# Kernel optimization log

Measured on AMD Instinct MI355X. Metric: run time of the kernel, lower is better.

## Reference

```python
import jax, jax.numpy as jnp
import numpy as np


def _lstm_cell(x, h, c, W_ih, b_ih, W_hh, b_hh):
    # PyTorch gate order: i, f, g, o
    gates = x @ W_ih.T + b_ih + h @ W_hh.T + b_hh
    i, f, g, o = jnp.split(gates, 4, axis=-1)
    c = jax.nn.sigmoid(f) * c + jax.nn.sigmoid(i) * jnp.tanh(g)
    h = jax.nn.sigmoid(o) * jnp.tanh(c)
    return h, c


def setup_inputs() -> dict:
    key = jax.random.key(0)
    ks = jax.random.split(key, 12)
    B, CR, PR = 8192, 168, 24
    E, I, H = 20, 3, 40  # embedding_size, input_size, hidden_size
    s = 0.1
    return {
        "z1": jax.random.normal(ks[0], (B, CR, 1), jnp.float32),
        "xc": jax.random.normal(ks[1], (B, CR + PR, I), jnp.float32),
        "W_emb": jax.random.normal(ks[2], (E, 1), jnp.float32) * s,
        "b_emb": jax.random.normal(ks[3], (E,), jnp.float32) * s,
        "W_ih": jax.random.normal(ks[4], (4 * H, E + I), jnp.float32) * s,
        "b_ih": jax.random.normal(ks[5], (4 * H,), jnp.float32) * s,
        "W_hh": jax.random.normal(ks[6], (4 * H, H), jnp.float32) * s,
        "b_hh": jax.random.normal(ks[7], (4 * H,), jnp.float32) * s,
        "W_mu": jax.random.normal(ks[8], (1, H), jnp.float32) * s,
        "b_mu": jax.random.normal(ks[9], (1,), jnp.float32) * s,
        "W_sig": jax.random.normal(ks[10], (1, H), jnp.float32) * s,
        "b_sig": jax.random.normal(ks[11], (1,), jnp.float32) * s,
        "conditioning_range": 168,
        "prediction_range": 24,
    }


def reference(z1, xc, W_emb, b_emb, W_ih, b_ih, W_hh, b_hh, W_mu, b_mu, W_sig, b_sig, conditioning_range, prediction_range):
    B = z1.shape[0]
    H = W_hh.shape[1]
    v = jnp.mean(z1, axis=1, keepdims=True) + 1.0  # [B,1,1] scale factor
    v2 = v[:, 0, :]                                # [B,1]

    # ---- conditioning phase: t = 1 .. CR-1 ----
    emb_cond = (z1[:, : conditioning_range - 1, :] / v) @ W_emb.T + b_emb  # [B,CR-1,E]
    xs = jnp.concatenate([emb_cond, xc[:, 1:conditioning_range, :]], axis=-1)
    xs = jnp.swapaxes(xs, 0, 1)  # [T,B,E+I]
    h0 = jnp.zeros((B, H), z1.dtype)
    c0 = jnp.zeros((B, H), z1.dtype)

    def cond_step(carry, x_t):
        h, c = carry
        h, c = _lstm_cell(x_t, h, c, W_ih, b_ih, W_hh, b_hh)
        return (h, c), None

    (h, c), _ = jax.lax.scan(cond_step, (h0, c0), xs)

    eps = jax.random.normal(jax.random.key(42), (prediction_range, B, 1), z1.dtype)
    xc_pred = jnp.swapaxes(
        xc[:, conditioning_range: conditioning_range + prediction_range, :], 0, 1
    )  # [PR,B,I]

    def pred_step(carry, inp):
        h, c, y = carry
        x_t, e_t = inp
        emb = (y / v2) @ W_emb.T + b_emb                       # [B,E]
        h, c = _lstm_cell(jnp.concatenate([emb, x_t], axis=-1), h, c, W_ih, b_ih, W_hh, b_hh)
        mu = h @ W_mu.T + b_mu                                 # [B,1]
        sigma = jax.nn.softplus(h @ W_sig.T + b_sig)           # [B,1]
        y = jax.lax.stop_gradient(mu + sigma * e_t)            # Normal.sample (no grad)
        return (h, c, y), (y * v2, mu * v2, sigma * v2)

    y0 = z1[:, -1, :]  # [B,1]
    _, (outs, mus, sigmas) = jax.lax.scan(pred_step, (h, c, y0), (xc_pred, eps))

    outputs = jnp.swapaxes(outs, 0, 1)[..., :]   # [B,PR,1]
    mus = jnp.swapaxes(mus, 0, 1)
    sigmas = jnp.swapaxes(sigmas, 0, 1)
    return outputs, mus, sigmas
```

## Files before the change

### kernel.cpp

```cpp
#include <hip/hip_runtime.h>

#define B_TOTAL   8192
#define CR_LEN    168
#define PR_LEN    24
#define HID       40
#define ROWS      6
#define NTHREADS  256
#define OUT_STRIDE (B_TOTAL * PR_LEN)

__device__ __forceinline__ float fast_rcp(float x) { return __builtin_amdgcn_rcpf(x); }

__device__ __forceinline__ float sigmoid_f(float x) {
    return fast_rcp(1.0f + __expf(-x));
}

__device__ __forceinline__ float tanh_f(float x) {
    float ax = fabsf(x);
    float e  = __expf(-2.0f * ax);
    float r  = (1.0f - e) * fast_rcp(1.0f + e);
    return copysignf(r, x);
}

__device__ __forceinline__ unsigned rotl32(unsigned x, int d) {
    return (x << d) | (x >> (32 - d));
}

__device__ __forceinline__ void threefry2x32(unsigned k0, unsigned k1,
                                             unsigned c0, unsigned c1,
                                             unsigned& o0, unsigned& o1) {
    const unsigned k2 = 0x1BD11BDAu ^ k0 ^ k1;
    unsigned x0 = c0 + k0, x1 = c1 + k1;
#define TF_R(rr) { x0 += x1; x1 = rotl32(x1, (rr)); x1 ^= x0; }
    TF_R(13) TF_R(15) TF_R(26) TF_R(6)  x0 += k1; x1 += k2 + 1u;
    TF_R(17) TF_R(29) TF_R(16) TF_R(24) x0 += k2; x1 += k0 + 2u;
    TF_R(13) TF_R(15) TF_R(26) TF_R(6)  x0 += k0; x1 += k1 + 3u;
    TF_R(17) TF_R(29) TF_R(16) TF_R(24) x0 += k1; x1 += k2 + 4u;
    TF_R(13) TF_R(15) TF_R(26) TF_R(6)  x0 += k2; x1 += k0 + 5u;
#undef TF_R
    o0 = x0; o1 = x1;
}

__device__ __forceinline__ float erfinv_f(float x) {
    float w = -__logf(fmaf(-x, x, 1.0f));
    float p;
    if (w < 5.0f) {
        w -= 2.5f;
        p = 2.81022636e-08f;
        p = fmaf(p, w, 3.43273939e-07f);
        p = fmaf(p, w, -3.5233877e-06f);
        p = fmaf(p, w, -4.39150654e-06f);
        p = fmaf(p, w, 0.00021858087f);
        p = fmaf(p, w, -0.00125372503f);
        p = fmaf(p, w, -0.00417768164f);
        p = fmaf(p, w, 0.246640727f);
        p = fmaf(p, w, 1.50140941f);
    } else {
        w = sqrtf(w) - 3.0f;
        p = -0.000200214257f;
        p = fmaf(p, w, 0.000100950558f);
        p = fmaf(p, w, 0.00134934322f);
        p = fmaf(p, w, -0.00367342844f);
        p = fmaf(p, w, 0.00573950773f);
        p = fmaf(p, w, -0.0076224613f);
        p = fmaf(p, w, 0.00943887047f);
        p = fmaf(p, w, 1.00167406f);
        p = fmaf(p, w, 2.83297682f);
    }
    return p * x;
}

__device__ __forceinline__ float kat_poison() {
    float poison = 0.0f;
    unsigned o0, o1;
    threefry2x32(0u, 0u, 0u, 0u, o0, o1);
    bool ok1 = (o0 == 0x6b200159u) && (o1 == 0x99ba4efeu);
    threefry2x32(0xFFFFFFFFu, 0xFFFFFFFFu, 0xFFFFFFFFu, 0xFFFFFFFFu, o0, o1);
    bool ok2 = (o0 == 0x1cb996fcu) && (o1 == 0xbb002be7u);
    if (!(ok1 && ok2)) poison += 4096.0f;
    threefry2x32(0x13198a2eu, 0x03707344u, 0x243f6a88u, 0x85a308d3u, o0, o1);
    bool ok3 = (o0 == 0xc4923a9cu) && (o1 == 0x483df7a0u);
    if (!ok3) poison += 8192.0f;
    return poison;
}

#define DOT4(acc, w4, h4) \
    acc = fmaf((w4).x, (h4).x, acc); acc = fmaf((w4).y, (h4).y, acc); \
    acc = fmaf((w4).z, (h4).z, acc); acc = fmaf((w4).w, (h4).w, acc);

#define LSTM_STEP(z1n, xa, xb, xv, hptr) do {                                  \
    float a0 = fmaf(fA0, (z1n), fC0); float a1 = fmaf(fA1, (z1n), fC1);        \
    float a2 = fmaf(fA2, (z1n), fC2); float a3 = fmaf(fA3, (z1n), fC3);        \
    a0 = fmaf(fp00, (xa), a0); a1 = fmaf(fp01, (xa), a1);                      \
    a2 = fmaf(fp02, (xa), a2); a3 = fmaf(fp03, (xa), a3);                      \
    a0 = fmaf(fp10, (xb), a0); a1 = fmaf(fp11, (xb), a1);                      \
    a2 = fmaf(fp12, (xb), a2); a3 = fmaf(fp13, (xb), a3);                      \
    a0 = fmaf(fp20, (xv), a0); a1 = fmaf(fp21, (xv), a1);                      \
    a2 = fmaf(fp22, (xv), a2); a3 = fmaf(fp23, (xv), a3);                      \
    float4 h4;                                                                 \
    h4 = ((const float4*)(hptr))[0];                                           \
    DOT4(a0, wA0, h4) DOT4(a1, wB0, h4) DOT4(a2, wC0, h4) DOT4(a3, wD0, h4)    \
    h4 = ((const float4*)(hptr))[1];                                           \
    DOT4(a0, wA1, h4) DOT4(a1, wB1, h4) DOT4(a2, wC1, h4) DOT4(a3, wD1, h4)    \
    h4 = ((const float4*)(hptr))[2];                                           \
    DOT4(a0, wA2, h4) DOT4(a1, wB2, h4) DOT4(a2, wC2, h4) DOT4(a3, wD2, h4)    \
    h4 = ((const float4*)(hptr))[3];                                           \
    DOT4(a0, wA3, h4) DOT4(a1, wB3, h4) DOT4(a2, wC3, h4) DOT4(a3, wD3, h4)    \
    h4 = ((const float4*)(hptr))[4];                                           \
    DOT4(a0, wA4, h4) DOT4(a1, wB4, h4) DOT4(a2, wC4, h4) DOT4(a3, wD4, h4)    \
    h4 = ((const float4*)(hptr))[5];                                           \
    DOT4(a0, wA5, h4) DOT4(a1, wB5, h4) DOT4(a2, wC5, h4) DOT4(a3, wD5, h4)    \
    h4 = ((const float4*)(hptr))[6];                                           \
    DOT4(a0, wA6, h4) DOT4(a1, wB6, h4) DOT4(a2, wC6, h4) DOT4(a3, wD6, h4)    \
    h4 = ((const float4*)(hptr))[7];                                           \
    DOT4(a0, wA7, h4) DOT4(a1, wB7, h4) DOT4(a2, wC7, h4) DOT4(a3, wD7, h4)    \
    h4 = ((const float4*)(hptr))[8];                                           \
    DOT4(a0, wA8, h4) DOT4(a1, wB8, h4) DOT4(a2, wC8, h4) DOT4(a3, wD8, h4)    \
    h4 = ((const float4*)(hptr))[9];                                           \
    DOT4(a0, wA9, h4) DOT4(a1, wB9, h4) DOT4(a2, wC9, h4) DOT4(a3, wD9, h4)    \
    float gi = sigmoid_f(a0);                                                  \
    float gf = sigmoid_f(a1);                                                  \
    float gg = tanh_f(a2);                                                     \
    float go = sigmoid_f(a3);                                                  \
    c_st = fmaf(gf, c_st, gi * gg);                                            \
    h_st = go * tanh_f(c_st);                                                  \
} while (0)

#define LOADW(P, base)                                                         \
    const float4 P##0 = pw[(base) + 0], P##1 = pw[(base) + 1],                 \
                 P##2 = pw[(base) + 2], P##3 = pw[(base) + 3],                 \
                 P##4 = pw[(base) + 4], P##5 = pw[(base) + 5],                 \
                 P##6 = pw[(base) + 6], P##7 = pw[(base) + 7],                 \
                 P##8 = pw[(base) + 8], P##9 = pw[(base) + 9];

#define XCOEF(g, fAv, fCv, f0v, f1v, f2v) {                                    \
    const int row_ = (g) * HID + j;                                            \
    const float* wr_ = W_ih + row_ * 23;                                       \
    float a_ = 0.0f, cc_ = b_ih[row_] + b_hh[row_];                            \
    _Pragma("unroll")                                                          \
    for (int e = 0; e < 20; e++) {                                             \
        float wv_ = wr_[e];                                                    \
        a_  = fmaf(wv_, W_emb[e], a_);                                         \
        cc_ = fmaf(wv_, b_emb[e], cc_);                                        \
    }                                                                          \
    fAv = a_; fCv = cc_; f0v = wr_[20]; f1v = wr_[21]; f2v = wr_[22];          \
}

__launch_bounds__(NTHREADS, 1)
__global__ void deepar_kernel(const float* __restrict__ z1,
                              const float* __restrict__ xc,
                              const float* __restrict__ W_emb,
                              const float* __restrict__ b_emb,
                              const float* __restrict__ W_ih,
                              const float* __restrict__ b_ih,
                              const float* __restrict__ W_hh,
                              const float* __restrict__ b_hh,
                              const float* __restrict__ W_mu,
                              const float* __restrict__ b_mu,
                              const float* __restrict__ W_sig,
                              const float* __restrict__ b_sig,
                              float* __restrict__ out) {
    __shared__ __align__(16) float z1_s[ROWS][CR_LEN];
    __shared__ __align__(16) float xc_s[ROWS][(CR_LEN + PR_LEN) * 3];
    __shared__ __align__(16) float h_s[2][ROWS][HID];
    __shared__ float eps_s[ROWS][PR_LEN];
    __shared__ float y_s[ROWS];
    __shared__ __align__(16) float wmu_s[HID];
    __shared__ __align__(16) float wsg_s[HID];
    __shared__ float bmu_s, bsg_s;

    const int tid = threadIdx.x;
    const int r   = tid / HID;
    const int j   = tid % HID;
    const int b0  = blockIdx.x * ROWS;
    const int b   = b0 + r;
    const bool active = (r < ROWS) && (b < B_TOTAL);

    {
        int nrow = B_TOTAL - b0;
        if (nrow > ROWS) nrow = ROWS;
        if (nrow < 0) nrow = 0;
        const float4* s1 = (const float4*)(z1 + (size_t)b0 * CR_LEN);
        float4* d1 = (float4*)&z1_s[0][0];
        const int n1 = nrow * (CR_LEN / 4);
        for (int idx = tid; idx < n1; idx += NTHREADS) d1[idx] = s1[idx];
        const float4* s2 = (const float4*)(xc + (size_t)b0 * (CR_LEN + PR_LEN) * 3);
        float4* d2 = (float4*)&xc_s[0][0];
        const int n2 = nrow * ((CR_LEN + PR_LEN) * 3 / 4);
        for (int idx = tid; idx < n2; idx += NTHREADS) d2[idx] = s2[idx];
    }
    if (tid < HID)                 wmu_s[tid] = W_mu[tid];
    else if (tid < 2 * HID)        wsg_s[tid - HID] = W_sig[tid - HID];
    else if (tid == 2 * HID)       bmu_s = b_mu[0];
    else if (tid == 2 * HID + 1)   bsg_s = b_sig[0];

    const float4* pw = (const float4*)W_hh;
    LOADW(wA, (0 * HID + j) * 10)
    LOADW(wB, (1 * HID + j) * 10)
    LOADW(wC, (2 * HID + j) * 10)
    LOADW(wD, (3 * HID + j) * 10)

    float fA0, fA1, fA2, fA3, fC0, fC1, fC2, fC3;
    float fp00, fp01, fp02, fp03, fp10, fp11, fp12, fp13, fp20, fp21, fp22, fp23;
    XCOEF(0, fA0, fC0, fp00, fp10, fp20)
    XCOEF(1, fA1, fC1, fp01, fp11, fp21)
    XCOEF(2, fA2, fC2, fp02, fp12, fp22)
    XCOEF(3, fA3, fC3, fp03, fp13, fp23)

    __syncthreads();

    float v = 0.0f, inv_v = 0.0f;
    if (active) {
        float s = 0.0f;
#pragma unroll
        for (int q = 0; q < CR_LEN / 4; q++) {
            float4 zz = *(const float4*)&z1_s[r][4 * q];
            s += zz.x + zz.y + zz.z + zz.w;
        }
        v = s * (1.0f / (float)CR_LEN) + 1.0f;
        inv_v = 1.0f / v;
    }

    if (active && j < PR_LEN) {
        unsigned i = (unsigned)j * B_TOTAL + (unsigned)b;
        unsigned o0, o1;
        threefry2x32(0u, 42u, 0u, i, o0, o1);
        unsigned bits = o0 ^ o1;
        float f = __uint_as_float((bits >> 9) | 0x3F800000u) - 1.0f;
        const float lo = -0.99999994f;
        float u = fmaxf(lo, fmaf(f, 2.0f, lo));
        eps_s[r][j] = 1.41421356237f * erfinv_f(u);
    }

    if (active) { h_s[0][r][j] = 0.0f; }
    float c_st = 0.0f, h_st = 0.0f;
    __syncthreads();

    int cur = 0;

    for (int t = 0; t < CR_LEN - 1; t++) {
        if (active) {
            float z1n = z1_s[r][t] * inv_v;
            float xa = xc_s[r][3 * (t + 1) + 0];
            float xb = xc_s[r][3 * (t + 1) + 1];
            float xv = xc_s[r][3 * (t + 1) + 2];
            LSTM_STEP(z1n, xa, xb, xv, &h_s[cur][r][0]);
            h_s[cur ^ 1][r][j] = h_st;
        }
        __syncthreads();
        cur ^= 1;
    }

    if (active && j == 0) y_s[r] = z1_s[r][CR_LEN - 1];
    __syncthreads();

    for (int t = 0; t < PR_LEN; t++) {
        if (active) {
            float z1n = y_s[r] * inv_v;
            float xa = xc_s[r][3 * (CR_LEN + t) + 0];
            float xb = xc_s[r][3 * (CR_LEN + t) + 1];
            float xv = xc_s[r][3 * (CR_LEN + t) + 2];
            LSTM_STEP(z1n, xa, xb, xv, &h_s[cur][r][0]);
            h_s[cur ^ 1][r][j] = h_st;
        }
        __syncthreads();
        cur ^= 1;
        if (active && j == 0) {
            float mu = bmu_s, sp = bsg_s;
#pragma unroll
            for (int q = 0; q < 10; q++) {
                float4 h4 = *(const float4*)&h_s[cur][r][4 * q];
                float4 wm = *(const float4*)&wmu_s[4 * q];
                float4 ws = *(const float4*)&wsg_s[4 * q];
                mu = fmaf(wm.x, h4.x, mu); mu = fmaf(wm.y, h4.y, mu);
                mu = fmaf(wm.z, h4.z, mu); mu = fmaf(wm.w, h4.w, mu);
                sp = fmaf(ws.x, h4.x, sp); sp = fmaf(ws.y, h4.y, sp);
                sp = fmaf(ws.z, h4.z, sp); sp = fmaf(ws.w, h4.w, sp);
            }
            float sigma = fmaxf(sp, 0.0f) + log1pf(__expf(-fabsf(sp)));
            float y = fmaf(sigma, eps_s[r][t], mu);
            y_s[r] = y;
            const int ob = b * PR_LEN + t;
            float poison = (b == 0 && t == 0) ? kat_poison() : 0.0f;
            out[ob]                  = y * v + poison;
            out[OUT_STRIDE + ob]     = mu * v;
            out[2 * OUT_STRIDE + ob] = sigma * v;
        }
        __syncthreads();
    }
}

extern "C" void kernel_launch(void* const* d_in, const int* in_sizes, int n_in,
                              void* d_out, int out_size, void* d_ws, size_t ws_size,
                              hipStream_t stream) {
    const float* z1    = (const float*)d_in[0];
    const float* xc    = (const float*)d_in[1];
    const float* W_emb = (const float*)d_in[2];
    const float* b_emb = (const float*)d_in[3];
    const float* W_ih  = (const float*)d_in[4];
    const float* b_ih  = (const float*)d_in[5];
    const float* W_hh  = (const float*)d_in[6];
    const float* b_hh  = (const float*)d_in[7];
    const float* W_mu  = (const float*)d_in[8];
    const float* b_mu  = (const float*)d_in[9];
    const float* W_sig = (const float*)d_in[10];
    const float* b_sig = (const float*)d_in[11];
    float* out = (float*)d_out;

    dim3 grid((B_TOTAL + ROWS - 1) / ROWS);
    dim3 block(NTHREADS);
    deepar_kernel<<<grid, block, 0, stream>>>(z1, xc, W_emb, b_emb, W_ih, b_ih,
                                              W_hh, b_hh, W_mu, b_mu, W_sig, b_sig,
                                              out);
}
```

Measured before the change: 487.0 us.

## Process two batch rows per thread to reuse register-resident W_hh weights

Each thread now computes its hidden unit for two batch rows at once, so the 160 W_hh weights held in registers serve two dot products per load of h. A block covers 16 rows with 320 threads instead of 6 rows with 256 threads (only 240 of which were active), which gives 512 blocks instead of 1366. The idea is to raise arithmetic per weight register and per barrier and to remove idle lanes. The costs are more live registers (two accumulator sets and two cell states), fewer blocks to spread over the CUs, and an extra barrier per prediction step for the output head.

```diff
diff --git a/kernel.cpp b/kernel.cpp
--- a/kernel.cpp
+++ b/kernel.cpp
@@ -4,8 +4,10 @@
 #define CR_LEN    168
 #define PR_LEN    24
 #define HID       40
-#define ROWS      6
-#define NTHREADS  256
+#define PAIRS     8
+#define ROWS      16
+#define NTHREADS  320
+#define XC_LEN    ((CR_LEN + PR_LEN) * 3)
 #define OUT_STRIDE (B_TOTAL * PR_LEN)
 
 __device__ __forceinline__ float fast_rcp(float x) { return __builtin_amdgcn_rcpf(x); }
@@ -87,42 +89,12 @@
     acc = fmaf((w4).x, (h4).x, acc); acc = fmaf((w4).y, (h4).y, acc); \
     acc = fmaf((w4).z, (h4).z, acc); acc = fmaf((w4).w, (h4).w, acc);
 
-#define LSTM_STEP(z1n, xa, xb, xv, hptr) do {                                  \
-    float a0 = fmaf(fA0, (z1n), fC0); float a1 = fmaf(fA1, (z1n), fC1);        \
-    float a2 = fmaf(fA2, (z1n), fC2); float a3 = fmaf(fA3, (z1n), fC3);        \
-    a0 = fmaf(fp00, (xa), a0); a1 = fmaf(fp01, (xa), a1);                      \
-    a2 = fmaf(fp02, (xa), a2); a3 = fmaf(fp03, (xa), a3);                      \
-    a0 = fmaf(fp10, (xb), a0); a1 = fmaf(fp11, (xb), a1);                      \
-    a2 = fmaf(fp12, (xb), a2); a3 = fmaf(fp13, (xb), a3);                      \
-    a0 = fmaf(fp20, (xv), a0); a1 = fmaf(fp21, (xv), a1);                      \
-    a2 = fmaf(fp22, (xv), a2); a3 = fmaf(fp23, (xv), a3);                      \
-    float4 h4;                                                                 \
-    h4 = ((const float4*)(hptr))[0];                                           \
-    DOT4(a0, wA0, h4) DOT4(a1, wB0, h4) DOT4(a2, wC0, h4) DOT4(a3, wD0, h4)    \
-    h4 = ((const float4*)(hptr))[1];                                           \
-    DOT4(a0, wA1, h4) DOT4(a1, wB1, h4) DOT4(a2, wC1, h4) DOT4(a3, wD1, h4)    \
-    h4 = ((const float4*)(hptr))[2];                                           \
-    DOT4(a0, wA2, h4) DOT4(a1, wB2, h4) DOT4(a2, wC2, h4) DOT4(a3, wD2, h4)    \
-    h4 = ((const float4*)(hptr))[3];                                           \
-    DOT4(a0, wA3, h4) DOT4(a1, wB3, h4) DOT4(a2, wC3, h4) DOT4(a3, wD3, h4)    \
-    h4 = ((const float4*)(hptr))[4];                                           \
-    DOT4(a0, wA4, h4) DOT4(a1, wB4, h4) DOT4(a2, wC4, h4) DOT4(a3, wD4, h4)    \
-    h4 = ((const float4*)(hptr))[5];                                           \
-    DOT4(a0, wA5, h4) DOT4(a1, wB5, h4) DOT4(a2, wC5, h4) DOT4(a3, wD5, h4)    \
-    h4 = ((const float4*)(hptr))[6];                                           \
-    DOT4(a0, wA6, h4) DOT4(a1, wB6, h4) DOT4(a2, wC6, h4) DOT4(a3, wD6, h4)    \
-    h4 = ((const float4*)(hptr))[7];                                           \
-    DOT4(a0, wA7, h4) DOT4(a1, wB7, h4) DOT4(a2, wC7, h4) DOT4(a3, wD7, h4)    \
-    h4 = ((const float4*)(hptr))[8];                                           \
-    DOT4(a0, wA8, h4) DOT4(a1, wB8, h4) DOT4(a2, wC8, h4) DOT4(a3, wD8, h4)    \
-    h4 = ((const float4*)(hptr))[9];                                           \
-    DOT4(a0, wA9, h4) DOT4(a1, wB9, h4) DOT4(a2, wC9, h4) DOT4(a3, wD9, h4)    \
-    float gi = sigmoid_f(a0);                                                  \
-    float gf = sigmoid_f(a1);                                                  \
-    float gg = tanh_f(a2);                                                     \
-    float go = sigmoid_f(a3);                                                  \
-    c_st = fmaf(gf, c_st, gi * gg);                                            \
-    h_st = go * tanh_f(c_st);                                                  \
+#define QSTEP(q) do {                                                          \
+    float4 h4A = hpA[q]; float4 h4B = hpB[q];                                  \
+    DOT4(a0, wA##q, h4A) DOT4(b0, wA##q, h4B)                                  \
+    DOT4(a1, wB##q, h4A) DOT4(b1, wB##q, h4B)                                  \
+    DOT4(a2, wC##q, h4A) DOT4(b2, wC##q, h4B)                                  \
+    DOT4(a3, wD##q, h4A) DOT4(b3, wD##q, h4B)                                  \
 } while (0)
 
 #define LOADW(P, base)                                                         \
@@ -144,6 +116,62 @@
     }                                                                          \
     fAv = a_; fCv = cc_; f0v = wr_[20]; f1v = wr_[21]; f2v = wr_[22];          \
 }
+
+#define LSTM2_STEP(zn0, xa0, xb0, xv0, zn1, xa1, xb1, xv1) do {                \
+    float a0 = fmaf(fA0, (zn0), fC0), a1 = fmaf(fA1, (zn0), fC1);              \
+    float a2 = fmaf(fA2, (zn0), fC2), a3 = fmaf(fA3, (zn0), fC3);              \
+    float b0 = fmaf(fA0, (zn1), fC0), b1 = fmaf(fA1, (zn1), fC1);              \
+    float b2 = fmaf(fA2, (zn1), fC2), b3 = fmaf(fA3, (zn1), fC3);              \
+    a0 = fmaf(fp00, (xa0), a0); a1 = fmaf(fp01, (xa0), a1);                    \
+    a2 = fmaf(fp02, (xa0), a2); a3 = fmaf(fp03, (xa0), a3);                    \
+    b0 = fmaf(fp00, (xa1), b0); b1 = fmaf(fp01, (xa1), b1);                    \
+    b2 = fmaf(fp02, (xa1), b2); b3 = fmaf(fp03, (xa1), b3);                    \
+    a0 = fmaf(fp10, (xb0), a0); a1 = fmaf(fp11, (xb0), a1);                    \
+    a2 = fmaf(fp12, (xb0), a2); a3 = fmaf(fp13, (xb0), a3);                    \
+    b0 = fmaf(fp10, (xb1), b0); b1 = fmaf(fp11, (xb1), b1);                    \
+    b2 = fmaf(fp12, (xb1), b2); b3 = fmaf(fp13, (xb1), b3);                    \
+    a0 = fmaf(fp20, (xv0), a0); a1 = fmaf(fp21, (xv0), a1);                    \
+    a2 = fmaf(fp22, (xv0), a2); a3 = fmaf(fp23, (xv0), a3);                    \
+    b0 = fmaf(fp20, (xv1), b0); b1 = fmaf(fp21, (xv1), b1);                    \
+    b2 = fmaf(fp22, (xv1), b2); b3 = fmaf(fp23, (xv1), b3);                    \
+    const float4* hpA = (const float4*)&h_s[cur][r0][0];                       \
+    const float4* hpB = (const float4*)&h_s[cur][r1][0];                       \
+    QSTEP(0); QSTEP(1); QSTEP(2); QSTEP(3); QSTEP(4);                          \
+    QSTEP(5); QSTEP(6); QSTEP(7); QSTEP(8); QSTEP(9);                          \
+    float gi0 = sigmoid_f(a0), gf0 = sigmoid_f(a1);                            \
+    float gg0 = tanh_f(a2),    go0 = sigmoid_f(a3);                            \
+    c0_st = fmaf(gf0, c0_st, gi0 * gg0);                                       \
+    h_s[cur ^ 1][r0][j] = go0 * tanh_f(c0_st);                                 \
+    float gi1 = sigmoid_f(b0), gf1 = sigmoid_f(b1);                            \
+    float gg1 = tanh_f(b2),    go1 = sigmoid_f(b3);                            \
+    c1_st = fmaf(gf1, c1_st, gi1 * gg1);                                       \
+    h_s[cur ^ 1][r1][j] = go1 * tanh_f(c1_st);                                 \
+} while (0)
+
+#define HEAD(rr, t) do {                                                       \
+    const int bglob_ = b_base + (rr);                                          \
+    float mu = bmu_s, sp = bsg_s;                                              \
+    const float4* hp_ = (const float4*)&h_s[cur ^ 1][rr][0];                   \
+    _Pragma("unroll")                                                          \
+    for (int q = 0; q < 10; q++) {                                             \
+        float4 h4 = hp_[q];                                                    \
+        float4 wm = *(const float4*)&wmu_s[4 * q];                             \
+        float4 ws = *(const float4*)&wsg_s[4 * q];                             \
+        mu = fmaf(wm.x, h4.x, mu); mu = fmaf(wm.y, h4.y, mu);                  \
+        mu = fmaf(wm.z, h4.z, mu); mu = fmaf(wm.w, h4.w, mu);                  \
+        sp = fmaf(ws.x, h4.x, sp); sp = fmaf(ws.y, h4.y, sp);                  \
+        sp = fmaf(ws.z, h4.z, sp); sp = fmaf(ws.w, h4.w, sp);                  \
+    }                                                                          \
+    float sigma = fmaxf(sp, 0.0f) + log1pf(__expf(-fabsf(sp)));               \
+    float y = fmaf(sigma, eps_s[rr][t], mu);                                   \
+    y_s[rr] = y;                                                               \
+    const float vv = v_s[rr];                                                  \
+    const int ob = bglob_ * PR_LEN + (t);                                      \
+    float poison = (bglob_ == 0 && (t) == 0) ? kat_poison() : 0.0f;            \
+    out[ob]                  = y * vv + poison;                                \
+    out[OUT_STRIDE + ob]     = mu * vv;                                        \
+    out[2 * OUT_STRIDE + ob] = sigma * vv;                                     \
+} while (0)
 
 __launch_bounds__(NTHREADS, 1)
 __global__ void deepar_kernel(const float* __restrict__ z1,
@@ -160,44 +188,33 @@
                               const float* __restrict__ b_sig,
                               float* __restrict__ out) {
     __shared__ __align__(16) float z1_s[ROWS][CR_LEN];
-    __shared__ __align__(16) float xc_s[ROWS][(CR_LEN + PR_LEN) * 3];
+    __shared__ __align__(16) float xc_s[ROWS][XC_LEN];
     __shared__ __align__(16) float h_s[2][ROWS][HID];
     __shared__ float eps_s[ROWS][PR_LEN];
     __shared__ float y_s[ROWS];
+    __shared__ float v_s[ROWS], iv_s[ROWS];
     __shared__ __align__(16) float wmu_s[HID];
     __shared__ __align__(16) float wsg_s[HID];
     __shared__ float bmu_s, bsg_s;
 
     const int tid = threadIdx.x;
-    const int r   = tid / HID;
-    const int j   = tid % HID;
-    const int b0  = blockIdx.x * ROWS;
-    const int b   = b0 + r;
-    const bool active = (r < ROWS) && (b < B_TOTAL);
+    const int p   = tid / HID;
+    const int j   = tid - p * HID;
+    const int r0  = 2 * p, r1 = 2 * p + 1;
+    const int b_base = blockIdx.x * ROWS;
 
     {
-        int nrow = B_TOTAL - b0;
-        if (nrow > ROWS) nrow = ROWS;
-        if (nrow < 0) nrow = 0;
-        const float4* s1 = (const float4*)(z1 + (size_t)b0 * CR_LEN);
+        const float4* s1 = (const float4*)(z1 + (size_t)b_base * CR_LEN);
         float4* d1 = (float4*)&z1_s[0][0];
-        const int n1 = nrow * (CR_LEN / 4);
-        for (int idx = tid; idx < n1; idx += NTHREADS) d1[idx] = s1[idx];
-        const float4* s2 = (const float4*)(xc + (size_t)b0 * (CR_LEN + PR_LEN) * 3);
+        for (int idx = tid; idx < ROWS * (CR_LEN / 4); idx += NTHREADS) d1[idx] = s1[idx];
+        const float4* s2 = (const float4*)(xc + (size_t)b_base * XC_LEN);
         float4* d2 = (float4*)&xc_s[0][0];
-        const int n2 = nrow * ((CR_LEN + PR_LEN) * 3 / 4);
-        for (int idx = tid; idx < n2; idx += NTHREADS) d2[idx] = s2[idx];
+        for (int idx = tid; idx < ROWS * (XC_LEN / 4); idx += NTHREADS) d2[idx] = s2[idx];
     }
     if (tid < HID)                 wmu_s[tid] = W_mu[tid];
     else if (tid < 2 * HID)        wsg_s[tid - HID] = W_sig[tid - HID];
     else if (tid == 2 * HID)       bmu_s = b_mu[0];
     else if (tid == 2 * HID + 1)   bsg_s = b_sig[0];
-
-    const float4* pw = (const float4*)W_hh;
-    LOADW(wA, (0 * HID + j) * 10)
-    LOADW(wB, (1 * HID + j) * 10)
-    LOADW(wC, (2 * HID + j) * 10)
-    LOADW(wD, (3 * HID + j) * 10)
 
     float fA0, fA1, fA2, fA3, fC0, fC1, fC2, fC3;
     float fp00, fp01, fp02, fp03, fp10, fp11, fp12, fp13, fp20, fp21, fp22, fp23;
@@ -206,86 +223,66 @@
     XCOEF(2, fA2, fC2, fp02, fp12, fp22)
     XCOEF(3, fA3, fC3, fp03, fp13, fp23)
 
+    const float4* pw = (const float4*)W_hh;
+    LOADW(wA, (0 * HID + j) * 10)
+    LOADW(wB, (1 * HID + j) * 10)
+    LOADW(wC, (2 * HID + j) * 10)
+    LOADW(wD, (3 * HID + j) * 10)
+
     __syncthreads();
 
-    float v = 0.0f, inv_v = 0.0f;
-    if (active) {
+    if (tid < ROWS) {
         float s = 0.0f;
 #pragma unroll
         for (int q = 0; q < CR_LEN / 4; q++) {
-            float4 zz = *(const float4*)&z1_s[r][4 * q];
+            float4 zz = *(const float4*)&z1_s[tid][4 * q];
             s += zz.x + zz.y + zz.z + zz.w;
         }
-        v = s * (1.0f / (float)CR_LEN) + 1.0f;
-        inv_v = 1.0f / v;
-    }
-
-    if (active && j < PR_LEN) {
-        unsigned i = (unsigned)j * B_TOTAL + (unsigned)b;
+        float v = s * (1.0f / (float)CR_LEN) + 1.0f;
+        v_s[tid]  = v;
+        iv_s[tid] = 1.0f / v;
+    }
+
+    for (int idx = tid; idx < ROWS * PR_LEN; idx += NTHREADS) {
+        const int row_ = idx / PR_LEN;
+        const int tt   = idx - row_ * PR_LEN;
+        unsigned i = (unsigned)tt * B_TOTAL + (unsigned)(b_base + row_);
         unsigned o0, o1;
         threefry2x32(0u, 42u, 0u, i, o0, o1);
         unsigned bits = o0 ^ o1;
         float f = __uint_as_float((bits >> 9) | 0x3F800000u) - 1.0f;
         const float lo = -0.99999994f;
-        float u = fmaxf(lo, fmaf(f, 2.0f, lo));
-        eps_s[r][j] = 1.41421356237f * erfinv_f(u);
-    }
-
-    if (active) { h_s[0][r][j] = 0.0f; }
-    float c_st = 0.0f, h_st = 0.0f;
+        float uu = fmaxf(lo, fmaf(f, 2.0f, lo));
+        eps_s[row_][tt] = 1.41421356237f * erfinv_f(uu);
+    }
+
+    h_s[0][r0][j] = 0.0f;
+    h_s[0][r1][j] = 0.0f;
+    float c0_st = 0.0f, c1_st = 0.0f;
     __syncthreads();
 
+    const float iv0 = iv_s[r0], iv1 = iv_s[r1];
     int cur = 0;
 
     for (int t = 0; t < CR_LEN - 1; t++) {
-        if (active) {
-            float z1n = z1_s[r][t] * inv_v;
-            float xa = xc_s[r][3 * (t + 1) + 0];
-            float xb = xc_s[r][3 * (t + 1) + 1];
-            float xv = xc_s[r][3 * (t + 1) + 2];
-            LSTM_STEP(z1n, xa, xb, xv, &h_s[cur][r][0]);
-            h_s[cur ^ 1][r][j] = h_st;
-        }
+        const int xo = 3 * (t + 1);
+        LSTM2_STEP(z1_s[r0][t] * iv0, xc_s[r0][xo], xc_s[r0][xo + 1], xc_s[r0][xo + 2],
+                   z1_s[r1][t] * iv1, xc_s[r1][xo], xc_s[r1][xo + 1], xc_s[r1][xo + 2]);
         __syncthreads();
         cur ^= 1;
     }
 
-    if (active && j == 0) y_s[r] = z1_s[r][CR_LEN - 1];
+    if (j == 0) { y_s[r0] = z1_s[r0][CR_LEN - 1]; y_s[r1] = z1_s[r1][CR_LEN - 1]; }
     __syncthreads();
 
     for (int t = 0; t < PR_LEN; t++) {
-        if (active) {
-            float z1n = y_s[r] * inv_v;
-            float xa = xc_s[r][3 * (CR_LEN + t) + 0];
-            float xb = xc_s[r][3 * (CR_LEN + t) + 1];
-            float xv = xc_s[r][3 * (CR_LEN + t) + 2];
-            LSTM_STEP(z1n, xa, xb, xv, &h_s[cur][r][0]);
-            h_s[cur ^ 1][r][j] = h_st;
-        }
+        const int xo = 3 * (CR_LEN + t);
+        LSTM2_STEP(y_s[r0] * iv0, xc_s[r0][xo], xc_s[r0][xo + 1], xc_s[r0][xo + 2],
+                   y_s[r1] * iv1, xc_s[r1][xo], xc_s[r1][xo + 1], xc_s[r1][xo + 2]);
+        __syncthreads();
+        if (j == 0) { HEAD(r0, t); HEAD(r1, t); }
         __syncthreads();
         cur ^= 1;
-        if (active && j == 0) {
-            float mu = bmu_s, sp = bsg_s;
-#pragma unroll
-            for (int q = 0; q < 10; q++) {
-                float4 h4 = *(const float4*)&h_s[cur][r][4 * q];
-                float4 wm = *(const float4*)&wmu_s[4 * q];
-                float4 ws = *(const float4*)&wsg_s[4 * q];
-                mu = fmaf(wm.x, h4.x, mu); mu = fmaf(wm.y, h4.y, mu);
-                mu = fmaf(wm.z, h4.z, mu); mu = fmaf(wm.w, h4.w, mu);
-                sp = fmaf(ws.x, h4.x, sp); sp = fmaf(ws.y, h4.y, sp);
-                sp = fmaf(ws.z, h4.z, sp); sp = fmaf(ws.w, h4.w, sp);
-            }
-            float sigma = fmaxf(sp, 0.0f) + log1pf(__expf(-fabsf(sp)));
-            float y = fmaf(sigma, eps_s[r][t], mu);
-            y_s[r] = y;
-            const int ob = b * PR_LEN + t;
-            float poison = (b == 0 && t == 0) ? kat_poison() : 0.0f;
-            out[ob]                  = y * v + poison;
-            out[OUT_STRIDE + ob]     = mu * v;
-            out[2 * OUT_STRIDE + ob] = sigma * v;
-        }
-        __syncthreads();
     }
 }
 
@@ -306,7 +303,7 @@
     const float* b_sig = (const float*)d_in[11];
     float* out = (float*)d_out;
 
-    dim3 grid((B_TOTAL + ROWS - 1) / ROWS);
+    dim3 grid(B_TOTAL / ROWS);
     dim3 block(NTHREADS);
     deepar_kernel<<<grid, block, 0, stream>>>(z1, xc, W_emb, b_emb, W_ih, b_ih,
                                               W_hh, b_hh, W_mu, b_mu, W_sig, b_sig,
```

After: 904.0 us. +85.6%, slower.
